# Performance work log

Measured on AMD Instinct MI355X. Metric: run time of the kernel, lower is better.

## Reference

```python
import jax, jax.numpy as jnp
import numpy as np

NHEAD = 16
EPS = 1e-6

def _phi_norm(x):
    # phi = silu, then L2 normalize over last dim (torch F.normalize: x / max(||x||, eps))
    x = jax.nn.silu(x)
    n = jnp.linalg.norm(x, axis=-1, keepdims=True)
    return x / jnp.maximum(n, EPS)

def setup_inputs() -> dict:
    key = jax.random.key(0)
    k1, k2, k3 = jax.random.split(key, 3)
    B, M, N, D = 4, 1024, 2048, 1024
    q = jax.random.normal(k1, (B, M, D), dtype=jnp.float32)
    kv = jax.random.normal(k2, (B, N, D), dtype=jnp.float32)
    kv_mask = jax.random.bernoulli(k3, 0.1, (B, N))  # True = masked out
    return {"q": q, "kv": kv, "kv_mask": kv_mask}

def reference(q, kv, kv_mask):
    B, M, D = q.shape
    N = kv.shape[1]
    dh = D // NHEAD
    # [B, H, M, dh] / [B, H, N, dh]
    qh = q.reshape(B, M, NHEAD, dh).transpose(0, 2, 1, 3)
    kh = kv.reshape(B, N, NHEAD, dh).transpose(0, 2, 1, 3)
    vh = kh  # values are raw kv heads (no phi/norm)
    qh_n = _phi_norm(qh)
    kh_n = _phi_norm(kh)
    scores = jnp.einsum('bhmd,bhnd->bhmn', qh_n, kh_n) / jnp.sqrt(jnp.asarray(dh, qh_n.dtype))
    scores = jnp.where(kv_mask[:, None, None, :], -jnp.inf, scores)
    attn = jax.nn.softmax(scores.astype(jnp.float32), axis=-1).astype(scores.dtype)
    out = jnp.einsum('bhmn,bhnd->bhmd', attn, vh)
    return out.transpose(0, 2, 1, 3).reshape(B, M, D)
```

## Files before the change

kernel.cpp:

```cpp
#include <hip/hip_runtime.h>
#include <hip/hip_bf16.h>
#include <cmath>
#include <stdint.h>

#define B_ 4
#define M_ 1024
#define N_ 2048
#define D_ 1024
#define H_ 16
#define DH_ 64
#define NT 64
#define NTH 16
#define PITCH 72

typedef __bf16 bf16_t;
typedef __attribute__((ext_vector_type(8))) __bf16 bf16x8;
typedef __attribute__((ext_vector_type(16))) float f32x16;
typedef __attribute__((ext_vector_type(2))) float f32x2;

static __device__ __forceinline__ float silu_f(float x) {
  return x / (1.0f + __expf(-x));
}

static __device__ __forceinline__ unsigned pk2(float a, float b) {
  union { __bf16 h[2]; unsigned u; } p;
  p.h[0] = (__bf16)a; p.h[1] = (__bf16)b;
  return p.u;
}

static __device__ __forceinline__ void gload16(const bf16_t* g, bf16_t* l) {
  typedef __attribute__((address_space(1))) const unsigned GU;
  typedef __attribute__((address_space(3))) unsigned LU;
  __builtin_amdgcn_global_load_lds((GU*)(const unsigned*)g, (LU*)(unsigned*)l,
                                   16, 0, 0);
}

static __device__ __forceinline__ int sw23(int x) {
  return (x & ~12) | ((x & 4) << 1) | ((x & 8) >> 1);
}

__global__ __launch_bounds__(256) void prep_kernel(
    const float* __restrict__ kv, const int* __restrict__ kv_mask,
    bf16_t* __restrict__ kp, bf16_t* __restrict__ vt,
    unsigned long long* __restrict__ mb) {
  __shared__ __align__(16) bf16_t Lt[NT][PITCH];
  const int bx = blockIdx.x;
  const int hp = bx & 7;
  const int nt = (bx >> 3) & 31;
  const int b  = bx >> 8;
  const int n0 = nt * NT;
  const int tid = threadIdx.x;
  const float keep = kv_mask[b * N_ + n0 + (tid >> 2)] ? 0.f : 1.f;

  #pragma unroll
  for (int hi = 0; hi < 2; ++hi) {
    const int h = hp * 2 + hi;
    const size_t bh = (size_t)(b * H_ + h);
    {
      const int r = tid >> 2, c0 = (tid & 3) * 16;
      const float* src = kv + ((size_t)(b * N_ + n0 + r)) * D_ + h * DH_ + c0;
      union { float f[16]; float4 v4[4]; } raw;
      raw.v4[0] = *(const float4*)(src + 0);
      raw.v4[1] = *(const float4*)(src + 4);
      raw.v4[2] = *(const float4*)(src + 8);
      raw.v4[3] = *(const float4*)(src + 12);
      float sv[16];
      float ss = 0.f;
      #pragma unroll
      for (int i = 0; i < 16; ++i) { sv[i] = silu_f(raw.f[i]); ss += sv[i] * sv[i]; }
      ss += __shfl_xor(ss, 1); ss += __shfl_xor(ss, 2);
      const float inv = keep / fmaxf(sqrtf(ss), 1e-6f);
      union { bf16_t bs[16]; uint4 u[2]; } pk;
      #pragma unroll
      for (int i = 0; i < 16; ++i) pk.bs[i] = (bf16_t)(sv[i] * inv);
      const size_t fbase = bh * 131072 +
          (size_t)((nt * 8 + (r >> 5) * 4 + (tid & 3)) * 512 + sw23(r & 31) * 8);
      *(uint4*)(kp + fbase)       = pk.u[0];
      *(uint4*)(kp + fbase + 256) = pk.u[1];
      union { bf16_t bs[16]; uint4 u[2]; } pv;
      #pragma unroll
      for (int i = 0; i < 16; ++i) pv.bs[i] = (bf16_t)(raw.f[i] * keep);
      uint4* ldst = (uint4*)&Lt[r][c0];
      ldst[0] = pv.u[0]; ldst[1] = pv.u[1];
    }
    __syncthreads();
    {
      const int d = tid >> 2, nc = (tid & 3) * 16;
      union { bf16_t bs[16]; uint4 u[2]; } pk;
      #pragma unroll
      for (int i = 0; i < 16; ++i) pk.bs[i] = Lt[nc + i][d];
      uint4* dst = (uint4*)(vt + (bh * DH_ + d) * N_ + n0 + nc);
      dst[0] = pk.u[0]; dst[1] = pk.u[1];
    }
    __syncthreads();
  }
  if (bx == 0 && tid < B_ * (N_ / 64)) {
    const int b2 = tid >> 5, tt = tid & 31;
    unsigned long long m = 0ull;
    for (int i = 0; i < 64; ++i)
      if (kv_mask[b2 * N_ + tt * 64 + i]) m |= (1ull << i);
    mb[tid] = m;
  }
}

__global__ __launch_bounds__(512, 4) void attn_kernel(
    const float* __restrict__ q, const bf16_t* __restrict__ kp,
    const bf16_t* __restrict__ vt, const unsigned long long* __restrict__ mb,
    float* __restrict__ out) {
  __shared__ __align__(1024) char smem[33280];

  const int tid  = threadIdx.x;
  const int w    = tid >> 6;
  const int wq   = w & 3;
  const int half = w >> 2;
  const int lane = tid & 63;
  const int l31  = lane & 31;
  const int hi   = lane >> 5;
  const int rho  = l31 & 7;

  const int wg = (blockIdx.x & 7) * 64 + (blockIdx.x >> 3);
  const int bh = wg >> 3;
  const int m0 = (wg & 7) * 128;
  const int b = bh >> 4, h = bh & 15;

  const bf16_t* vtb = vt + (size_t)bh * DH_ * N_;
  const bf16_t* kfb = kp + (size_t)bh * 131072 + (size_t)half * 65536
                         + (size_t)lane * 8;

  const int srow  = lane >> 3;
  const int sslot = (lane & 7) ^ srow;
  const bf16_t* vs0 = vtb + (size_t)(wq * 16 + srow) * N_ + half * NTH * NT + sslot * 8;
  const bf16_t* vs1 = vs0 + 8 * N_;

  {
    bf16_t* Vd = (bf16_t*)(smem + (half * 2 + 0) * 8192) + wq * 16 * NT;
    gload16(vs0, Vd); gload16(vs1, Vd + 512);
  }
  bf16x8 ka[2][4];
  #pragma unroll
  for (int nb = 0; nb < 2; ++nb)
    #pragma unroll
    for (int kk = 0; kk < 4; ++kk)
      ka[nb][kk] = *(const bf16x8*)(kfb + (nb * 4 + kk) * 512);

  bf16x8 qb[4];
  {
    const float* qrow =
        q + ((size_t)(b * M_ + m0 + wq * 32 + l31)) * D_ + h * DH_ + hi * 8;
    float sv[32];
    float ss = 0.f;
    #pragma unroll
    for (int kk = 0; kk < 4; ++kk) {
      float4 a0 = *(const float4*)(qrow + kk * 16);
      float4 a1 = *(const float4*)(qrow + kk * 16 + 4);
      sv[kk * 8 + 0] = silu_f(a0.x); sv[kk * 8 + 1] = silu_f(a0.y);
      sv[kk * 8 + 2] = silu_f(a0.z); sv[kk * 8 + 3] = silu_f(a0.w);
      sv[kk * 8 + 4] = silu_f(a1.x); sv[kk * 8 + 5] = silu_f(a1.y);
      sv[kk * 8 + 6] = silu_f(a1.z); sv[kk * 8 + 7] = silu_f(a1.w);
      #pragma unroll
      for (int i = 0; i < 8; ++i) ss += sv[kk * 8 + i] * sv[kk * 8 + i];
    }
    ss += __shfl_xor(ss, 32);
    const float inv = 0.125f / fmaxf(sqrtf(ss), 1e-6f);
    #pragma unroll
    for (int kk = 0; kk < 4; ++kk) {
      union { unsigned u[4]; bf16x8 v; } pq;
      #pragma unroll
      for (int jj = 0; jj < 4; ++jj)
        pq.u[jj] = pk2(sv[kk * 8 + jj * 2] * inv, sv[kk * 8 + jj * 2 + 1] * inv);
      qb[kk] = pq.v;
    }
  }

  int foff[2][4];
  #pragma unroll
  for (int i = 0; i < 2; ++i)
    #pragma unroll
    for (int j = 0; j < 4; ++j)
      foff[i][j] = (i * 32 + l31) * 64 + ((((j << 1) + hi) ^ rho) << 3);

  f32x16 o0, o1, zvec;
  #pragma unroll
  for (int r = 0; r < 16; ++r) { o0[r] = 0.f; o1[r] = 0.f; zvec[r] = 0.f; }
  float lrun = 0.f;
  unsigned cl = 0, ch = 0;
  const unsigned long long* mbb = mb + b * (N_ / 64);

  for (int tt = 0; tt < NTH; ++tt) {
    __syncthreads();
    const int cur = tt & 1;
    if (tt + 1 < NTH) {
      const int nx = cur ^ 1;
      const size_t vo = (size_t)(tt + 1) * NT;
      bf16_t* Vd = (bf16_t*)(smem + (half * 2 + nx) * 8192) + wq * 16 * NT;
      gload16(vs0 + vo, Vd); gload16(vs1 + vo, Vd + 512);
    }
    const unsigned long long mk = mbb[half * NTH + tt];
    cl += (unsigned)__popcll(mk & 0x00FF00FF00FF00FFULL);
    ch += (unsigned)__popcll(mk & 0xFF00FF00FF00FF00ULL);

    const bf16_t* Vc = (const bf16_t*)(smem + (half * 2 + cur) * 8192);

    bf16x8 pa[4];
    #pragma unroll
    for (int nb = 0; nb < 2; ++nb) {
      __builtin_amdgcn_s_setprio(1);
      f32x16 s = __builtin_amdgcn_mfma_f32_32x32x16_bf16(
          ka[nb][0], qb[0], zvec, 0, 0, 0);
      #pragma unroll
      for (int kk = 1; kk < 4; ++kk)
        s = __builtin_amdgcn_mfma_f32_32x32x16_bf16(ka[nb][kk], qb[kk], s, 0, 0, 0);
      __builtin_amdgcn_s_setprio(0);

      f32x2 p2[8];
      #pragma unroll
      for (int i = 0; i < 8; ++i) {
        f32x2 x; x.x = s[2 * i]; x.y = s[2 * i + 1];
        f32x2 u = x * 0.5f + 1.0f;
        p2[i] = x * u + 1.0f;
      }
      f32x2 t0 = (p2[0] + p2[1]) + (p2[2] + p2[3]);
      f32x2 t1 = (p2[4] + p2[5]) + (p2[6] + p2[7]);
      f32x2 ts = t0 + t1;
      lrun += ts.x + ts.y;

      union { unsigned u[4]; bf16x8 v; } f0, f1;
      #pragma unroll
      for (int jj = 0; jj < 4; ++jj) {
        f0.u[jj] = pk2(p2[jj].x, p2[jj].y);
        f1.u[jj] = pk2(p2[4 + jj].x, p2[4 + jj].y);
      }
      pa[nb * 2]     = f0.v;
      pa[nb * 2 + 1] = f1.v;
    }

    {
      const bf16_t* kn = kfb + (size_t)((tt + 1) & 15) * 4096;
      #pragma unroll
      for (int nb = 0; nb < 2; ++nb)
        #pragma unroll
        for (int kk = 0; kk < 4; ++kk)
          ka[nb][kk] = *(const bf16x8*)(kn + (nb * 4 + kk) * 512);
    }

    __builtin_amdgcn_s_setprio(1);
    #pragma unroll
    for (int ks = 0; ks < 4; ++ks) {
      bf16x8 vb0 = *(const bf16x8*)(Vc + foff[0][ks]);
      bf16x8 vb1 = *(const bf16x8*)(Vc + foff[1][ks]);
      o0 = __builtin_amdgcn_mfma_f32_32x32x16_bf16(vb0, pa[ks], o0, 0, 0, 0);
      o1 = __builtin_amdgcn_mfma_f32_32x32x16_bf16(vb1, pa[ks], o1, 0, 0, 0);
    }
    __builtin_amdgcn_s_setprio(0);
  }

  lrun -= (float)(hi ? ch : cl);
  lrun += __shfl_xor(lrun, 32);

  __syncthreads();
  float* Ob = (float*)smem;
  float* Lb = (float*)(smem + 32768);

  if (half == 0) {
    #pragma unroll
    for (int r = 0; r < 16; ++r) {
      const int d = (r & 3) + ((r >> 2) << 3) + (hi << 2);
      Ob[d * 128 + wq * 32 + l31]        = o0[r];
      Ob[(d + 32) * 128 + wq * 32 + l31] = o1[r];
    }
    if (hi == 0) Lb[wq * 32 + l31] = lrun;
  }
  __syncthreads();
  if (half == 1) {
    #pragma unroll
    for (int r = 0; r < 16; ++r) {
      const int d = (r & 3) + ((r >> 2) << 3) + (hi << 2);
      Ob[d * 128 + wq * 32 + l31]        += o0[r];
      Ob[(d + 32) * 128 + wq * 32 + l31] += o1[r];
    }
    if (hi == 0) Lb[wq * 32 + l31] += lrun;
  }
  __syncthreads();
  {
    const int m = tid >> 2, dc = (tid & 3) * 16;
    const float lv = Lb[m];
    const float iv = lv > 0.f ? 1.0f / lv : 0.f;
    float* orow = out + ((size_t)(b * M_ + m0 + m)) * D_ + h * DH_ + dc;
    #pragma unroll
    for (int i0 = 0; i0 < 16; i0 += 4) {
      float4 v;
      v.x = Ob[(dc + i0 + 0) * 128 + m] * iv;
      v.y = Ob[(dc + i0 + 1) * 128 + m] * iv;
      v.z = Ob[(dc + i0 + 2) * 128 + m] * iv;
      v.w = Ob[(dc + i0 + 3) * 128 + m] * iv;
      *(float4*)(orow + i0) = v;
    }
  }
}

extern "C" void kernel_launch(void* const* d_in, const int* in_sizes, int n_in,
                              void* d_out, int out_size, void* d_ws, size_t ws_size,
                              hipStream_t stream) {
  const float* q  = (const float*)d_in[0];
  const float* kv = (const float*)d_in[1];
  const int* kv_mask = (const int*)d_in[2];
  float* out = (float*)d_out;

  bf16_t* kp = (bf16_t*)d_ws;
  bf16_t* vt = kp + (size_t)B_ * H_ * N_ * DH_;
  unsigned long long* mb =
      (unsigned long long*)((char*)d_ws + 2 * (size_t)B_ * H_ * N_ * DH_ * sizeof(bf16_t));

  prep_kernel<<<B_ * 32 * 8, 256, 0, stream>>>(kv, kv_mask, kp, vt, mb);
  attn_kernel<<<B_ * H_ * (M_ / 128), 512, 0, stream>>>(q, kp, vt, mb, out);
}
```

Before: 142.7 us.

## Pre-swizzle V into MFMA fragment layout and load directly to registers

```diff
diff --git a/kernel.cpp b/kernel.cpp
--- a/kernel.cpp
+++ b/kernel.cpp
@@ -26,13 +26,6 @@
   union { __bf16 h[2]; unsigned u; } p;
   p.h[0] = (__bf16)a; p.h[1] = (__bf16)b;
   return p.u;
-}
-
-static __device__ __forceinline__ void gload16(const bf16_t* g, bf16_t* l) {
-  typedef __attribute__((address_space(1))) const unsigned GU;
-  typedef __attribute__((address_space(3))) unsigned LU;
-  __builtin_amdgcn_global_load_lds((GU*)(const unsigned*)g, (LU*)(unsigned*)l,
-                                   16, 0, 0);
 }
 
 static __device__ __forceinline__ int sw23(int x) {
@@ -85,12 +78,18 @@
     }
     __syncthreads();
     {
-      const int d = tid >> 2, nc = (tid & 3) * 16;
-      union { bf16_t bs[16]; uint4 u[2]; } pk;
-      #pragma unroll
-      for (int i = 0; i < 16; ++i) pk.bs[i] = Lt[nc + i][d];
-      uint4* dst = (uint4*)(vt + (bh * DH_ + d) * N_ + n0 + nc);
-      dst[0] = pk.u[0]; dst[1] = pk.u[1];
+      const int f = tid >> 5;
+      const int i_ = f >> 2, ks = f & 3;
+      const int vl = tid & 31;
+      const int d = i_ * 32 + vl;
+      const size_t vbase = bh * 131072 + (size_t)((nt * 8 + f) * 512);
+      #pragma unroll
+      for (int hi2 = 0; hi2 < 2; ++hi2) {
+        union { bf16_t bs[8]; uint4 u; } vp;
+        #pragma unroll
+        for (int j = 0; j < 8; ++j) vp.bs[j] = Lt[ks * 16 + hi2 * 8 + j][d];
+        *(uint4*)(vt + vbase + (hi2 * 32 + vl) * 8) = vp.u;
+      }
     }
     __syncthreads();
   }
@@ -116,26 +115,17 @@
   const int lane = tid & 63;
   const int l31  = lane & 31;
   const int hi   = lane >> 5;
-  const int rho  = l31 & 7;
 
   const int wg = (blockIdx.x & 7) * 64 + (blockIdx.x >> 3);
   const int bh = wg >> 3;
   const int m0 = (wg & 7) * 128;
   const int b = bh >> 4, h = bh & 15;
 
-  const bf16_t* vtb = vt + (size_t)bh * DH_ * N_;
   const bf16_t* kfb = kp + (size_t)bh * 131072 + (size_t)half * 65536
                          + (size_t)lane * 8;
-
-  const int srow  = lane >> 3;
-  const int sslot = (lane & 7) ^ srow;
-  const bf16_t* vs0 = vtb + (size_t)(wq * 16 + srow) * N_ + half * NTH * NT + sslot * 8;
-  const bf16_t* vs1 = vs0 + 8 * N_;
-
-  {
-    bf16_t* Vd = (bf16_t*)(smem + (half * 2 + 0) * 8192) + wq * 16 * NT;
-    gload16(vs0, Vd); gload16(vs1, Vd + 512);
-  }
+  const bf16_t* vfb = vt + (size_t)bh * 131072 + (size_t)half * 65536
+                         + (size_t)lane * 8;
+
   bf16x8 ka[2][4];
   #pragma unroll
   for (int nb = 0; nb < 2; ++nb)
@@ -172,43 +162,28 @@
     }
   }
 
-  int foff[2][4];
+  f32x16 o0, o1;
   #pragma unroll
-  for (int i = 0; i < 2; ++i)
-    #pragma unroll
-    for (int j = 0; j < 4; ++j)
-      foff[i][j] = (i * 32 + l31) * 64 + ((((j << 1) + hi) ^ rho) << 3);
-
-  f32x16 o0, o1, zvec;
-  #pragma unroll
-  for (int r = 0; r < 16; ++r) { o0[r] = 0.f; o1[r] = 0.f; zvec[r] = 0.f; }
+  for (int r = 0; r < 16; ++r) { o0[r] = 0.f; o1[r] = 0.f; }
   float lrun = 0.f;
   unsigned cl = 0, ch = 0;
   const unsigned long long* mbb = mb + b * (N_ / 64);
 
+  #pragma unroll 1
   for (int tt = 0; tt < NTH; ++tt) {
-    __syncthreads();
-    const int cur = tt & 1;
-    if (tt + 1 < NTH) {
-      const int nx = cur ^ 1;
-      const size_t vo = (size_t)(tt + 1) * NT;
-      bf16_t* Vd = (bf16_t*)(smem + (half * 2 + nx) * 8192) + wq * 16 * NT;
-      gload16(vs0 + vo, Vd); gload16(vs1 + vo, Vd + 512);
-    }
     const unsigned long long mk = mbb[half * NTH + tt];
     cl += (unsigned)__popcll(mk & 0x00FF00FF00FF00FFULL);
     ch += (unsigned)__popcll(mk & 0xFF00FF00FF00FF00ULL);
 
-    const bf16_t* Vc = (const bf16_t*)(smem + (half * 2 + cur) * 8192);
-
     bf16x8 pa[4];
     #pragma unroll
     for (int nb = 0; nb < 2; ++nb) {
+      f32x16 s;
+      #pragma unroll
+      for (int r = 0; r < 16; ++r) s[r] = 0.f;
       __builtin_amdgcn_s_setprio(1);
-      f32x16 s = __builtin_amdgcn_mfma_f32_32x32x16_bf16(
-          ka[nb][0], qb[0], zvec, 0, 0, 0);
-      #pragma unroll
-      for (int kk = 1; kk < 4; ++kk)
+      #pragma unroll
+      for (int kk = 0; kk < 4; ++kk)
         s = __builtin_amdgcn_mfma_f32_32x32x16_bf16(ka[nb][kk], qb[kk], s, 0, 0, 0);
       __builtin_amdgcn_s_setprio(0);
 
@@ -234,6 +209,11 @@
       pa[nb * 2 + 1] = f1.v;
     }
 
+    const bf16_t* vfp = vfb + (size_t)tt * 4096;
+    bf16x8 va[4];
+    #pragma unroll
+    for (int ks = 0; ks < 4; ++ks)
+      va[ks] = *(const bf16x8*)(vfp + ks * 512);
     {
       const bf16_t* kn = kfb + (size_t)((tt + 1) & 15) * 4096;
       #pragma unroll
@@ -245,12 +225,17 @@
 
     __builtin_amdgcn_s_setprio(1);
     #pragma unroll
-    for (int ks = 0; ks < 4; ++ks) {
-      bf16x8 vb0 = *(const bf16x8*)(Vc + foff[0][ks]);
-      bf16x8 vb1 = *(const bf16x8*)(Vc + foff[1][ks]);
-      o0 = __builtin_amdgcn_mfma_f32_32x32x16_bf16(vb0, pa[ks], o0, 0, 0, 0);
-      o1 = __builtin_amdgcn_mfma_f32_32x32x16_bf16(vb1, pa[ks], o1, 0, 0, 0);
-    }
+    for (int ks = 0; ks < 4; ++ks)
+      o0 = __builtin_amdgcn_mfma_f32_32x32x16_bf16(va[ks], pa[ks], o0, 0, 0, 0);
+    __builtin_amdgcn_s_setprio(0);
+
+    #pragma unroll
+    for (int ks = 0; ks < 4; ++ks)
+      va[ks] = *(const bf16x8*)(vfp + (4 + ks) * 512);
+    __builtin_amdgcn_s_setprio(1);
+    #pragma unroll
+    for (int ks = 0; ks < 4; ++ks)
+      o1 = __builtin_amdgcn_mfma_f32_32x32x16_bf16(va[ks], pa[ks], o1, 0, 0, 0);
     __builtin_amdgcn_s_setprio(0);
   }
 
```

Result: slower. 146.1 us (+2.4%).
